# Kernel optimization log

Hardware: AMD Instinct MI355X
Metric: run time of the kernel (lower is better)

The kernel has to match this reference:

```python
import jax, jax.numpy as jnp
import numpy as np
import math

N_LAYERS = 6
D_MODEL = 1024
N_HEADS = 16
D_FF = 2 * D_MODEL  # PositionwiseFeedForward default argument=2
B, S = 4, 1024
EPS = 1e-6


def setup_inputs() -> dict:
    key = jax.random.key(0)
    ks = iter(jax.random.split(key, 40))
    sc = 0.02
    d, f, n = D_MODEL, D_FF, N_LAYERS
    inp = {
        "word_embed": jax.random.normal(next(ks), (B, S, d), dtype=jnp.float32),
        "mask": jnp.ones((B, S, S), dtype=jnp.int32),
        # per-layer attention projections (torch Linear convention: W [out,in])
        "wq": jax.random.normal(next(ks), (n, d, d), jnp.float32) * sc,
        "bq": jnp.zeros((n, d), jnp.float32),
        "wk": jax.random.normal(next(ks), (n, d, d), jnp.float32) * sc,
        "bk": jnp.zeros((n, d), jnp.float32),
        "wv": jax.random.normal(next(ks), (n, d, d), jnp.float32) * sc,
        "bv": jnp.zeros((n, d), jnp.float32),
        "wo": jax.random.normal(next(ks), (n, d, d), jnp.float32) * sc,
        "bo": jnp.zeros((n, d), jnp.float32),
        # per-layer FFN
        "w1": jax.random.normal(next(ks), (n, f, d), jnp.float32) * sc,
        "b1": jnp.zeros((n, f), jnp.float32),
        "w2": jax.random.normal(next(ks), (n, d, f), jnp.float32) * sc,
        "b2": jnp.zeros((n, d), jnp.float32),
        # per-layer sublayer LayerNorms + final norm
        "ln1a": jnp.ones((n, d), jnp.float32), "ln1b": jnp.zeros((n, d), jnp.float32),
        "ln2a": jnp.ones((n, d), jnp.float32), "ln2b": jnp.zeros((n, d), jnp.float32),
        "lnfa": jnp.ones((d,), jnp.float32), "lnfb": jnp.zeros((d,), jnp.float32),
    }
    return inp


def _layernorm(x, a, b):
    # matches torch module: std is unbiased (ddof=1), and divides by (std + eps)
    mean = jnp.mean(x, axis=-1, keepdims=True)
    std = jnp.std(x, axis=-1, keepdims=True, ddof=1)
    return a * (x - mean) / (std + EPS) + b


def _mha(x, mask, wq, bq, wk, bk, wv, bv, wo, bo):
    b, s, d = x.shape
    h, dk = N_HEADS, d // N_HEADS
    q = (x @ wq.T + bq).reshape(b, s, h, dk).transpose(0, 2, 1, 3)
    k = (x @ wk.T + bk).reshape(b, s, h, dk).transpose(0, 2, 1, 3)
    v = (x @ wv.T + bv).reshape(b, s, h, dk).transpose(0, 2, 1, 3)
    scores = jnp.einsum('bhqd,bhkd->bhqk', q, k) / math.sqrt(dk)  # [B,h,S,S]
    scores = jnp.where(mask[:, None, :, :] == 0, -1e9, scores)
    p = jax.nn.softmax(scores, axis=-1)
    o = jnp.einsum('bhqk,bhkd->bhqd', p, v)
    o = o.transpose(0, 2, 1, 3).reshape(b, s, d)
    return o @ wo.T + bo


def _ffn(x, w1, b1, w2, b2):
    return jax.nn.relu(x @ w1.T + b1) @ w2.T + b2


def reference(word_embed, mask, wq, bq, wk, bk, wv, bv, wo, bo,
              w1, b1, w2, b2, ln1a, ln1b, ln2a, ln2b, lnfa, lnfb):
    x = word_embed
    for i in range(N_LAYERS):
        # pre-norm residual sublayers (dropout = identity at eval)
        x = x + _mha(_layernorm(x, ln1a[i], ln1b[i]), mask,
                     wq[i], bq[i], wk[i], bk[i], wv[i], bv[i], wo[i], bo[i])
        x = x + _ffn(_layernorm(x, ln2a[i], ln2b[i]), w1[i], b1[i], w2[i], b2[i])
    return _layernorm(x, lnfa, lnfb)
```

## Files before the change

### kernel.cpp

```cpp
#include <hip/hip_runtime.h>

#define D_MODEL 1024
#define N_HEADS 16
#define DKH 64
#define D_FF 2048
#define N_LAYERS 6
#define BATCH 4
#define SEQ 1024
#define MROWS (BATCH*SEQ)

typedef unsigned short bf16_t;
using short8  = __attribute__((ext_vector_type(8))) short;
using floatx4 = __attribute__((ext_vector_type(4))) float;

__device__ __forceinline__ unsigned short f2bf(float f) {
    union { float f; unsigned int i; } v; v.f = f;
    unsigned int r = v.i + 0x7fffu + ((v.i >> 16) & 1u);
    return (unsigned short)(r >> 16);
}
__device__ __forceinline__ void gl2lds16(const void* g, void* l) {
    __builtin_amdgcn_global_load_lds(
        (const __attribute__((address_space(1))) unsigned int*)g,
        (__attribute__((address_space(3))) unsigned int*)l, 16, 0, 0);
}

__global__ __launch_bounds__(256) void wconv_kernel(const float* __restrict__ wq,
        const float* __restrict__ wk, const float* __restrict__ wv,
        const float* __restrict__ wo, const float* __restrict__ w1,
        const float* __restrict__ w2, bf16_t* __restrict__ dst) {
    const int e = (blockIdx.x * 256 + threadIdx.x) * 4;
    const float* src; int off;
    if (e < (1 << 22)) {
        const int seg = e >> 20;
        src = seg == 0 ? wq : seg == 1 ? wk : seg == 2 ? wv : wo;
        off = e & ((1 << 20) - 1);
    } else {
        const int e2 = e - (1 << 22);
        src = (e2 >> 21) ? w2 : w1;
        off = e2 & ((1 << 21) - 1);
    }
    const float4 v = *(const float4*)(src + off);
    ushort4 o; o.x = f2bf(v.x); o.y = f2bf(v.y); o.z = f2bf(v.z); o.w = f2bf(v.w);
    *(ushort4*)(dst + e) = o;
}

__device__ __forceinline__ float block_sum(float v, float* red) {
    __syncthreads();
    #pragma unroll
    for (int off = 32; off > 0; off >>= 1) v += __shfl_down(v, off, 64);
    int lane = threadIdx.x & 63, w = threadIdx.x >> 6;
    if (lane == 0) red[w] = v;
    __syncthreads();
    return red[0] + red[1] + red[2] + red[3];
}

template<bool BF16_OUT>
__global__ __launch_bounds__(256) void ln_kernel(const float* __restrict__ x,
        const float* __restrict__ gamma, const float* __restrict__ beta,
        void* __restrict__ outp) {
    __shared__ float red[4];
    const int row = blockIdx.x, t = threadIdx.x;
    float4 xv = ((const float4*)(x + (size_t)row * D_MODEL))[t];
    float mean = block_sum(xv.x + xv.y + xv.z + xv.w, red) * (1.0f / D_MODEL);
    float d0 = xv.x - mean, d1 = xv.y - mean, d2 = xv.z - mean, d3 = xv.w - mean;
    float ss = block_sum(d0*d0 + d1*d1 + d2*d2 + d3*d3, red);
    float inv = 1.0f / (sqrtf(ss * (1.0f / (D_MODEL - 1))) + 1e-6f);
    float4 g4 = ((const float4*)gamma)[t];
    float4 b4 = ((const float4*)beta)[t];
    float o0 = g4.x * (d0 * inv) + b4.x;
    float o1 = g4.y * (d1 * inv) + b4.y;
    float o2 = g4.z * (d2 * inv) + b4.z;
    float o3 = g4.w * (d3 * inv) + b4.w;
    if (BF16_OUT) {
        ushort4 o; o.x = f2bf(o0); o.y = f2bf(o1); o.z = f2bf(o2); o.w = f2bf(o3);
        ((ushort4*)outp)[(size_t)row * 256 + t] = o;
    } else {
        ((float4*)outp)[(size_t)row * 256 + t] = make_float4(o0, o1, o2, o3);
    }
}

template<int MODE>
__global__ __launch_bounds__(256) void mfma_gemm(const bf16_t* __restrict__ A,
        const bf16_t* __restrict__ W, const float* __restrict__ bias,
        const float* resid, void* Cp, int N, int K, int relu,
        const float* __restrict__ bias_k, const float* __restrict__ bias_v,
        void* Ck, void* Cvt) {
    __shared__ bf16_t As[2][128][32];
    __shared__ bf16_t Ws[2][128][32];
    const int tid = threadIdx.x, w = tid >> 6, lane = tid & 63;
    const int w32 = w * 32;
    const int m0 = blockIdx.y * 128, n0 = blockIdx.x * 128;
    const int wm = (w >> 1) * 64, wn = (w & 1) * 64;
    const bf16_t* ga = A + (size_t)(m0 + w32 + (lane >> 2)) * K + (lane & 3) * 8;
    const bf16_t* gw = W + (size_t)(n0 + w32 + (lane >> 2)) * K + (lane & 3) * 8;
    const int m_in = lane & 15;
    const int kq = (lane >> 4) * 8;
    floatx4 acc[4][4] = {};
#define STAGE(B) do { \
        gl2lds16(ga,          &As[B][w32][0]); \
        gl2lds16(ga + 16 * K, &As[B][w32 + 16][0]); \
        gl2lds16(gw,          &Ws[B][w32][0]); \
        gl2lds16(gw + 16 * K, &Ws[B][w32 + 16][0]); \
        ga += 32; gw += 32; } while (0)
    STAGE(0);
    int buf = 0;
    for (int k0 = 0; k0 < K; k0 += 32) {
        __syncthreads();
        if (k0 + 32 < K) STAGE(buf ^ 1);
        short8 af[4], bfr[4];
        #pragma unroll
        for (int i = 0; i < 4; i++) {
            af[i]  = *(const short8*)&As[buf][wm + i*16 + m_in][kq];
            bfr[i] = *(const short8*)&Ws[buf][wn + i*16 + m_in][kq];
        }
        #pragma unroll
        for (int mi = 0; mi < 4; mi++)
            #pragma unroll
            for (int ni = 0; ni < 4; ni++)
                acc[mi][ni] = __builtin_amdgcn_mfma_f32_16x16x32_bf16(
                    af[mi], bfr[ni], acc[mi][ni], 0, 0, 0);
        buf ^= 1;
    }
#undef STAGE
    const int rbase = m0 + wm + (lane >> 4) * 4;
    const int seg = (MODE == 3) ? (n0 >> 10) : 0;
    const float* bsel = (MODE == 3) ? (seg == 0 ? bias : seg == 1 ? bias_k : bias_v) : bias;
    #pragma unroll
    for (int ni = 0; ni < 4; ni++) {
        const int col  = n0 + wn + ni * 16 + m_in;
        const int colL = (MODE == 3) ? (col & 1023) : col;
        const float bv = bsel[colL];
        #pragma unroll
        for (int mi = 0; mi < 4; mi++) {
            const int row0 = rbase + mi * 16;
            if (MODE == 3 && seg == 2) {
                ushort4 o;
                o.x = f2bf(acc[mi][ni][0] + bv);
                o.y = f2bf(acc[mi][ni][1] + bv);
                o.z = f2bf(acc[mi][ni][2] + bv);
                o.w = f2bf(acc[mi][ni][3] + bv);
                *(ushort4*)((bf16_t*)Cvt + (size_t)colL * MROWS + row0) = o;
            } else {
                bf16_t* outb = (MODE == 3) ? (bf16_t*)(seg == 0 ? Cp : Ck) : (bf16_t*)Cp;
                #pragma unroll
                for (int r = 0; r < 4; r++) {
                    float v = acc[mi][ni][r] + bv;
                    if (MODE == 1 && relu) v = fmaxf(v, 0.f);
                    const size_t idx = (size_t)(row0 + r) * N + colL;
                    if (MODE == 0) {
                        float vo = v + (resid ? resid[idx] : 0.f);
                        ((float*)Cp)[idx] = vo;
                    } else {
                        outb[idx] = f2bf(v);
                    }
                }
            }
        }
    }
}

__global__ __launch_bounds__(256) void attn_mfma(const bf16_t* __restrict__ Q,
        const bf16_t* __restrict__ Kg, const bf16_t* __restrict__ Vt,
        bf16_t* __restrict__ Out) {
    __shared__ bf16_t KL[2][2][64][32];
    __shared__ bf16_t VL[2][2][64][32];
    __shared__ bf16_t Pl[4][16][72];
    const int qc = blockIdx.x, h = blockIdx.y, b = blockIdx.z;
    const int tid = threadIdx.x, w = tid >> 6, lane = tid & 63;
    const int w16 = w * 16;
    const int li = lane & 15, g = lane >> 4;

    const bf16_t* qp = Q + ((size_t)(b*SEQ + qc*64 + w16 + li)) * D_MODEL + h*DKH + g*8;
    short8 qf0 = *(const short8*)qp;
    short8 qf1 = *(const short8*)(qp + 32);

    const bf16_t* kg = Kg + ((size_t)(b*SEQ + w16 + (lane >> 2))) * D_MODEL
                          + h*DKH + (lane & 3) * 8;
    const bf16_t* vg = Vt + ((size_t)(h*DKH + w16 + (lane >> 2))) * MROWS
                          + b*SEQ + (lane & 3) * 8;

    floatx4 oacc[4] = {};
    float mrun = -3.0e38f, lrun = 0.0f;
#define ASTAGE(B) do { \
        gl2lds16(kg,      &KL[B][0][w16][0]); \
        gl2lds16(kg + 32, &KL[B][1][w16][0]); \
        gl2lds16(vg,      &VL[B][0][w16][0]); \
        gl2lds16(vg + 32, &VL[B][1][w16][0]); \
        kg += (size_t)64 * D_MODEL; vg += 64; } while (0)
    ASTAGE(0);
    int buf = 0;
    for (int kc = 0; kc < SEQ; kc += 64) {
        __syncthreads();
        if (kc + 64 < SEQ) ASTAGE(buf ^ 1);

        floatx4 st[4] = {};
        #pragma unroll
        for (int t = 0; t < 4; t++) {
            short8 ka0 = *(const short8*)&KL[buf][0][t*16 + li][g*8];
            short8 ka1 = *(const short8*)&KL[buf][1][t*16 + li][g*8];
            st[t] = __builtin_amdgcn_mfma_f32_16x16x32_bf16(ka0, qf0, st[t], 0, 0, 0);
            st[t] = __builtin_amdgcn_mfma_f32_16x16x32_bf16(ka1, qf1, st[t], 0, 0, 0);
        }
        float cm = -3.0e38f;
        #pragma unroll
        for (int t = 0; t < 4; t++)
            #pragma unroll
            for (int r = 0; r < 4; r++) {
                st[t][r] *= 0.125f;
                cm = fmaxf(cm, st[t][r]);
            }
        cm = fmaxf(cm, __shfl_xor(cm, 16, 64));
        cm = fmaxf(cm, __shfl_xor(cm, 32, 64));
        float mnew  = fmaxf(mrun, cm);
        float alpha = __expf(mrun - mnew);
        mrun = mnew;
        float psum = 0.0f;
        #pragma unroll
        for (int t = 0; t < 4; t++) {
            float e0 = __expf(st[t][0] - mnew);
            float e1 = __expf(st[t][1] - mnew);
            float e2 = __expf(st[t][2] - mnew);
            float e3 = __expf(st[t][3] - mnew);
            psum += (e0 + e1) + (e2 + e3);
            ushort4 pv; pv.x = f2bf(e0); pv.y = f2bf(e1); pv.z = f2bf(e2); pv.w = f2bf(e3);
            *(ushort4*)&Pl[w][li][t*16 + g*4] = pv;
        }
        psum += __shfl_xor(psum, 16, 64);
        psum += __shfl_xor(psum, 32, 64);
        lrun = lrun * alpha + psum;
        float a0 = __shfl(alpha, 4*g + 0, 64);
        float a1 = __shfl(alpha, 4*g + 1, 64);
        float a2 = __shfl(alpha, 4*g + 2, 64);
        float a3 = __shfl(alpha, 4*g + 3, 64);
        #pragma unroll
        for (int t = 0; t < 4; t++) {
            oacc[t][0] *= a0; oacc[t][1] *= a1; oacc[t][2] *= a2; oacc[t][3] *= a3;
        }
        short8 pa0 = *(const short8*)&Pl[w][li][g*8];
        short8 pa1 = *(const short8*)&Pl[w][li][32 + g*8];
        #pragma unroll
        for (int t = 0; t < 4; t++) {
            short8 vb0 = *(const short8*)&VL[buf][0][t*16 + li][g*8];
            short8 vb1 = *(const short8*)&VL[buf][1][t*16 + li][g*8];
            oacc[t] = __builtin_amdgcn_mfma_f32_16x16x32_bf16(pa0, vb0, oacc[t], 0, 0, 0);
            oacc[t] = __builtin_amdgcn_mfma_f32_16x16x32_bf16(pa1, vb1, oacc[t], 0, 0, 0);
        }
        buf ^= 1;
    }
#undef ASTAGE
    const float linv = 1.0f / lrun;
    float l0 = __shfl(linv, 4*g + 0, 64);
    float l1 = __shfl(linv, 4*g + 1, 64);
    float l2 = __shfl(linv, 4*g + 2, 64);
    float l3 = __shfl(linv, 4*g + 3, 64);
    const size_t row0 = (size_t)(b*SEQ + qc*64 + w16 + g*4);
    #pragma unroll
    for (int t = 0; t < 4; t++) {
        const int col = h*DKH + t*16 + li;
        Out[(row0 + 0) * D_MODEL + col] = f2bf(oacc[t][0] * l0);
        Out[(row0 + 1) * D_MODEL + col] = f2bf(oacc[t][1] * l1);
        Out[(row0 + 2) * D_MODEL + col] = f2bf(oacc[t][2] * l2);
        Out[(row0 + 3) * D_MODEL + col] = f2bf(oacc[t][3] * l3);
    }
}

extern "C" void kernel_launch(void* const* d_in, const int* in_sizes, int n_in,
                              void* d_out, int out_size, void* d_ws, size_t ws_size,
                              hipStream_t stream) {
    const float* we   = (const float*)d_in[0];
    const float* wq   = (const float*)d_in[2];
    const float* bq   = (const float*)d_in[3];
    const float* wk   = (const float*)d_in[4];
    const float* bk   = (const float*)d_in[5];
    const float* wv   = (const float*)d_in[6];
    const float* bv   = (const float*)d_in[7];
    const float* wo   = (const float*)d_in[8];
    const float* bo   = (const float*)d_in[9];
    const float* w1   = (const float*)d_in[10];
    const float* b1   = (const float*)d_in[11];
    const float* w2   = (const float*)d_in[12];
    const float* b2   = (const float*)d_in[13];
    const float* ln1a = (const float*)d_in[14];
    const float* ln1b = (const float*)d_in[15];
    const float* ln2a = (const float*)d_in[16];
    const float* ln2b = (const float*)d_in[17];
    const float* lnfa = (const float*)d_in[18];
    const float* lnfb = (const float*)d_in[19];

    char* ws8 = (char*)d_ws;
    const size_t MB = 1048576;
    float*  x   = (float*)(ws8);
    bf16_t* xnb = (bf16_t*)(ws8 + 16*MB);
    bf16_t* qb  = (bf16_t*)(ws8 + 24*MB);
    bf16_t* kbb = (bf16_t*)(ws8 + 32*MB);
    bf16_t* vtb = (bf16_t*)(ws8 + 40*MB);
    bf16_t* hb  = (bf16_t*)(ws8 + 24*MB);
    bf16_t* wb  = (bf16_t*)(ws8 + 48*MB);

    hipMemcpyAsync(x, we, 16*MB, hipMemcpyDeviceToDevice, stream);
    for (int l = 0; l < N_LAYERS; l++) {
        const size_t wOff = (size_t)l * D_MODEL * D_MODEL;
        const size_t fOff = (size_t)l * D_FF * D_MODEL;
        const size_t bOff = (size_t)l * D_MODEL;
        wconv_kernel<<<8192, 256, 0, stream>>>(wq + wOff, wk + wOff, wv + wOff,
                                               wo + wOff, w1 + fOff, w2 + fOff, wb);
        ln_kernel<true><<<MROWS, 256, 0, stream>>>(x, ln1a + bOff, ln1b + bOff, xnb);
        mfma_gemm<3><<<dim3(24, 32), 256, 0, stream>>>(xnb, wb, bq + bOff, nullptr, qb,
                1024, 1024, 0, bk + bOff, bv + bOff, kbb, vtb);
        attn_mfma<<<dim3(SEQ/64, N_HEADS, BATCH), 256, 0, stream>>>(qb, kbb, vtb, xnb);
        mfma_gemm<0><<<dim3(8, 32), 256, 0, stream>>>(xnb, wb + 3145728, bo + bOff, x, x,
                1024, 1024, 0, nullptr, nullptr, nullptr, nullptr);
        ln_kernel<true><<<MROWS, 256, 0, stream>>>(x, ln2a + bOff, ln2b + bOff, xnb);
        mfma_gemm<1><<<dim3(16, 32), 256, 0, stream>>>(xnb, wb + 4194304, b1 + (size_t)l*D_FF,
                nullptr, hb, 2048, 1024, 1, nullptr, nullptr, nullptr, nullptr);
        mfma_gemm<0><<<dim3(8, 32), 256, 0, stream>>>(hb, wb + 6291456, b2 + bOff, x, x,
                1024, 2048, 0, nullptr, nullptr, nullptr, nullptr);
    }
    ln_kernel<false><<<MROWS, 256, 0, stream>>>(x, lnfa, lnfb, (float*)d_out);
}
```

Measured before the change: 1.594 ms.

## Keep softmax probabilities in registers and swizzle K/V LDS tiles in attention

```diff
diff --git a/kernel.cpp b/kernel.cpp
--- a/kernel.cpp
+++ b/kernel.cpp
@@ -17,6 +17,11 @@
     union { float f; unsigned int i; } v; v.f = f;
     unsigned int r = v.i + 0x7fffu + ((v.i >> 16) & 1u);
     return (unsigned short)(r >> 16);
+}
+__device__ __forceinline__ unsigned int cvt_pk_bf16(float lo, float hi) {
+    unsigned int r;
+    asm("v_cvt_pk_bf16_f32 %0, %1, %2" : "=v"(r) : "v"(lo), "v"(hi));
+    return r;
 }
 __device__ __forceinline__ void gl2lds16(const void* g, void* l) {
     __builtin_amdgcn_global_load_lds(
@@ -145,6 +150,7 @@
                 #pragma unroll
                 for (int r = 0; r < 4; r++) {
                     float v = acc[mi][ni][r] + bv;
+                    if (MODE == 3 && seg == 0) v *= 0.125f;
                     if (MODE == 1 && relu) v = fmaxf(v, 0.f);
                     const size_t idx = (size_t)(row0 + r) * N + colL;
                     if (MODE == 0) {
@@ -164,7 +170,6 @@
         bf16_t* __restrict__ Out) {
     __shared__ bf16_t KL[2][2][64][32];
     __shared__ bf16_t VL[2][2][64][32];
-    __shared__ bf16_t Pl[4][16][72];
     const int qc = blockIdx.x, h = blockIdx.y, b = blockIdx.z;
     const int tid = threadIdx.x, w = tid >> 6, lane = tid & 63;
     const int w16 = w * 16;
@@ -174,10 +179,12 @@
     short8 qf0 = *(const short8*)qp;
     short8 qf1 = *(const short8*)(qp + 32);
 
+    const int swz = (((lane & 3) ^ ((lane >> 3) & 3))) * 8;
     const bf16_t* kg = Kg + ((size_t)(b*SEQ + w16 + (lane >> 2))) * D_MODEL
-                          + h*DKH + (lane & 3) * 8;
+                          + h*DKH + swz;
     const bf16_t* vg = Vt + ((size_t)(h*DKH + w16 + (lane >> 2))) * MROWS
-                          + b*SEQ + (lane & 3) * 8;
+                          + b*SEQ + swz;
+    const int ksw = (g ^ ((li >> 1) & 3)) * 8;
 
     floatx4 oacc[4] = {};
     float mrun = -3.0e38f, lrun = 0.0f;
@@ -196,8 +203,8 @@
         floatx4 st[4] = {};
         #pragma unroll
         for (int t = 0; t < 4; t++) {
-            short8 ka0 = *(const short8*)&KL[buf][0][t*16 + li][g*8];
-            short8 ka1 = *(const short8*)&KL[buf][1][t*16 + li][g*8];
+            short8 ka0 = *(const short8*)&KL[buf][0][t*16 + li][ksw];
+            short8 ka1 = *(const short8*)&KL[buf][1][t*16 + li][ksw];
             st[t] = __builtin_amdgcn_mfma_f32_16x16x32_bf16(ka0, qf0, st[t], 0, 0, 0);
             st[t] = __builtin_amdgcn_mfma_f32_16x16x32_bf16(ka1, qf1, st[t], 0, 0, 0);
         }
@@ -205,43 +212,63 @@
         #pragma unroll
         for (int t = 0; t < 4; t++)
             #pragma unroll
-            for (int r = 0; r < 4; r++) {
-                st[t][r] *= 0.125f;
+            for (int r = 0; r < 4; r++)
                 cm = fmaxf(cm, st[t][r]);
-            }
         cm = fmaxf(cm, __shfl_xor(cm, 16, 64));
         cm = fmaxf(cm, __shfl_xor(cm, 32, 64));
-        float mnew  = fmaxf(mrun, cm);
-        float alpha = __expf(mrun - mnew);
-        mrun = mnew;
+        if (!__all(cm <= mrun + 8.0f)) {
+            const float mnew  = fmaxf(mrun, cm);
+            const float alpha = __expf(mrun - mnew);
+            mrun = mnew;
+            lrun *= alpha;
+            const float a0 = __shfl(alpha, 4*g + 0, 64);
+            const float a1 = __shfl(alpha, 4*g + 1, 64);
+            const float a2 = __shfl(alpha, 4*g + 2, 64);
+            const float a3 = __shfl(alpha, 4*g + 3, 64);
+            #pragma unroll
+            for (int t = 0; t < 4; t++) {
+                oacc[t][0] *= a0; oacc[t][1] *= a1;
+                oacc[t][2] *= a2; oacc[t][3] *= a3;
+            }
+        }
         float psum = 0.0f;
+        unsigned int P2[4][2];
         #pragma unroll
         for (int t = 0; t < 4; t++) {
-            float e0 = __expf(st[t][0] - mnew);
-            float e1 = __expf(st[t][1] - mnew);
-            float e2 = __expf(st[t][2] - mnew);
-            float e3 = __expf(st[t][3] - mnew);
+            const float e0 = __expf(st[t][0] - mrun);
+            const float e1 = __expf(st[t][1] - mrun);
+            const float e2 = __expf(st[t][2] - mrun);
+            const float e3 = __expf(st[t][3] - mrun);
             psum += (e0 + e1) + (e2 + e3);
-            ushort4 pv; pv.x = f2bf(e0); pv.y = f2bf(e1); pv.z = f2bf(e2); pv.w = f2bf(e3);
-            *(ushort4*)&Pl[w][li][t*16 + g*4] = pv;
+            P2[t][0] = cvt_pk_bf16(e0, e1);
+            P2[t][1] = cvt_pk_bf16(e2, e3);
         }
         psum += __shfl_xor(psum, 16, 64);
         psum += __shfl_xor(psum, 32, 64);
-        lrun = lrun * alpha + psum;
-        float a0 = __shfl(alpha, 4*g + 0, 64);
-        float a1 = __shfl(alpha, 4*g + 1, 64);
-        float a2 = __shfl(alpha, 4*g + 2, 64);
-        float a3 = __shfl(alpha, 4*g + 3, 64);
+        lrun += psum;
+        const int ta = g >> 1;
+        const unsigned int xa0 = ta ? P2[1][0] : P2[0][0];
+        const unsigned int xa1 = ta ? P2[1][1] : P2[0][1];
+        const unsigned int xb0 = ta ? P2[3][0] : P2[2][0];
+        const unsigned int xb1 = ta ? P2[3][1] : P2[2][1];
+        const int la = li + ((lane & 16) << 1);
+        const int lb = la + 16;
+        union U4 { unsigned int u[4]; short8 s; };
+        U4 ua, ub;
+        ua.u[0] = (unsigned int)__shfl((int)xa0, la, 64);
+        ua.u[1] = (unsigned int)__shfl((int)xa1, la, 64);
+        ua.u[2] = (unsigned int)__shfl((int)xa0, lb, 64);
+        ua.u[3] = (unsigned int)__shfl((int)xa1, lb, 64);
+        ub.u[0] = (unsigned int)__shfl((int)xb0, la, 64);
+        ub.u[1] = (unsigned int)__shfl((int)xb1, la, 64);
+        ub.u[2] = (unsigned int)__shfl((int)xb0, lb, 64);
+        ub.u[3] = (unsigned int)__shfl((int)xb1, lb, 64);
+        const short8 pa0 = ua.s;
+        const short8 pa1 = ub.s;
         #pragma unroll
         for (int t = 0; t < 4; t++) {
-            oacc[t][0] *= a0; oacc[t][1] *= a1; oacc[t][2] *= a2; oacc[t][3] *= a3;
-        }
-        short8 pa0 = *(const short8*)&Pl[w][li][g*8];
-        short8 pa1 = *(const short8*)&Pl[w][li][32 + g*8];
-        #pragma unroll
-        for (int t = 0; t < 4; t++) {
-            short8 vb0 = *(const short8*)&VL[buf][0][t*16 + li][g*8];
-            short8 vb1 = *(const short8*)&VL[buf][1][t*16 + li][g*8];
+            short8 vb0 = *(const short8*)&VL[buf][0][t*16 + li][ksw];
+            short8 vb1 = *(const short8*)&VL[buf][1][t*16 + li][ksw];
             oacc[t] = __builtin_amdgcn_mfma_f32_16x16x32_bf16(pa0, vb0, oacc[t], 0, 0, 0);
             oacc[t] = __builtin_amdgcn_mfma_f32_16x16x32_bf16(pa1, vb1, oacc[t], 0, 0, 0);
         }
```

Measured after the change: 1.509 ms. 1.06x faster.
